# Kernel tuning notes

Hardware: AMD Instinct MI355X
Metric: run time of the kernel (lower is better)

The kernel has to match this reference:

```python
import jax, jax.numpy as jnp
import numpy as np
from jax import lax

R = 3                      # blob_r
S = 2 * R + 1              # 7: maxpool / neighborhood kernel size
THRESH = 0.997
PS_XY = 0.1                # vs_xy
PS_Z = 0.02                # vs_z
ZMIN = -2.0                # zrange[0]
K_PEAKS = 131072           # static upper bound replacing torch.nonzero

_offs = np.arange(S)
_gz, _gy, _gx = np.meshgrid(_offs, _offs, _offs, indexing='ij')  # patch axis order [z,y,x]
GZ = jnp.asarray(_gz.ravel(), dtype=jnp.int32)
GY = jnp.asarray(_gy.ravel(), dtype=jnp.int32)
GX = jnp.asarray(_gx.ravel(), dtype=jnp.int32)
# centroid filters: offsets -r..r along the matching patch axis (matches torch meshgrid layout)
FZ = jnp.asarray((_gz.ravel() - R).astype(np.float32))
FY = jnp.asarray((_gy.ravel() - R).astype(np.float32))
FX = jnp.asarray((_gx.ravel() - R).astype(np.float32))


def setup_inputs() -> dict:
    key = jax.random.key(0)
    pred_vol = jax.random.uniform(key, (1, 1, 128, 512, 512), dtype=jnp.float32)
    return {"pred_vol": pred_vol, "max_peaks": K_PEAKS}


def _forward(pred_vol, max_peaks):
    vol = pred_vol[0, 0]                               # [D,H,W]
    D, H, W = vol.shape
    thr = jnp.where(vol > THRESH, vol, 0.0)
    # MaxPool3d(kernel=2r+1, stride=1, padding=r) == SAME max window (pad with -inf)
    mp = lax.reduce_window(thr, -jnp.inf, lax.max, (S, S, S), (1, 1, 1), [(R, R)] * 3)
    conf = jnp.where((mp > 0.0) & (mp == thr), mp, 0.0)  # local maxima above threshold
    # fixed-size peak extraction (replaces torch.nonzero); zero-valued entries are padding
    vals, idx = lax.top_k(conf.reshape(-1), max_peaks)   # [K], [K]
    z = idx // (H * W)
    y = (idx % (H * W)) // W
    x = idx % W
    padv = jnp.pad(vol, R)                               # ConstantPad3d(r, 0)
    # gather (2r+1)^3 neighborhoods around each peak: [K, S^3]
    patches = padv[z[:, None] + GZ[None, :], y[:, None] + GY[None, :], x[:, None] + GX[None, :]]
    s0 = patches.sum(axis=1)                             # conv3d with ones filter == conf_rec sum
    xloc = jnp.einsum('kp,p->k', patches, FX) / s0
    yloc = jnp.einsum('kp,p->k', patches, FY) / s0
    zloc = jnp.einsum('kp,p->k', patches, FZ) / s0
    xf = x.astype(jnp.float32)
    yf = y.astype(jnp.float32)
    zf = z.astype(jnp.float32)
    xrec = (xf + xloc - (W - 1) / 2.0) * PS_XY
    yrec = (yf + yloc - (H - 1) / 2.0) * PS_XY
    zrec = (zf + zloc + 0.5) * PS_Z + ZMIN
    valid = vals > 0.0
    xyz = jnp.where(valid[:, None], jnp.stack((xrec, yrec, zrec), axis=1), 0.0)  # [K,3]
    out = jnp.concatenate([xyz, vals[:, None]], axis=1)  # [K,4] = (x,y,z,conf), padded rows are 0
    return out, valid


def reference(pred_vol, max_peaks):
    return _forward(pred_vol, max_peaks)
```

## Files before the change

kernel.cpp:

```cpp
#include <hip/hip_runtime.h>

#define DD 128
#define HH 512
#define WW 512
#define NVOX (DD*HH*WW)
#define THRESHV 0.997f
#define KPEAKS 131072
#define PEAK_CAP (1u<<18)
#define NBINS 65536


__global__ void k_init(unsigned* counters, unsigned* hist) {
    unsigned t = blockIdx.x * 1024u + threadIdx.x;
    if (t < 64) counters[t] = 0u;
    if (t < NBINS) hist[t] = 0u;
}

__global__ __launch_bounds__(512, 8)
void k_find(const float4* __restrict__ vol4, const float* __restrict__ vol,
            unsigned* counters, unsigned* hist,
            unsigned long long* keys, float4* psums) {
    __shared__ unsigned lcnt, pcnt, lbase;
    __shared__ unsigned cidx[384];
    __shared__ unsigned long long lbuf[192];
    __shared__ float4 sbuf[192];
    if (threadIdx.x == 0) { lcnt = 0; pcnt = 0; }
    __syncthreads();

    unsigned t = threadIdx.x;
    unsigned lane = t & 63u;
    unsigned w = t >> 6;
    unsigned blockBase4 = blockIdx.x * 2048u;

    unsigned b4 = blockBase4 + t;
    float4 a0 = vol4[b4];
    float4 a1 = vol4[b4 + 512u];
    float4 a2 = vol4[b4 + 1024u];
    float4 a3 = vol4[b4 + 1536u];
    __builtin_amdgcn_sched_barrier(0);
    unsigned m = 0u;
    m |= (a0.x > THRESHV ? 1u : 0u);
    m |= (a0.y > THRESHV ? 2u : 0u);
    m |= (a0.z > THRESHV ? 4u : 0u);
    m |= (a0.w > THRESHV ? 8u : 0u);
    m |= (a1.x > THRESHV ? 16u : 0u);
    m |= (a1.y > THRESHV ? 32u : 0u);
    m |= (a1.z > THRESHV ? 64u : 0u);
    m |= (a1.w > THRESHV ? 128u : 0u);
    m |= (a2.x > THRESHV ? 256u : 0u);
    m |= (a2.y > THRESHV ? 512u : 0u);
    m |= (a2.z > THRESHV ? 1024u : 0u);
    m |= (a2.w > THRESHV ? 2048u : 0u);
    m |= (a3.x > THRESHV ? 4096u : 0u);
    m |= (a3.y > THRESHV ? 8192u : 0u);
    m |= (a3.z > THRESHV ? 16384u : 0u);
    m |= (a3.w > THRESHV ? 32768u : 0u);
    while (m) {
        int b = __ffs(m) - 1;
        m &= m - 1u;
        unsigned f4 = blockBase4 + (unsigned)(b >> 2) * 512u + t;
        cidx[atomicAdd(&lcnt, 1u) & 383u] = f4 * 4u + (unsigned)(b & 3);
    }
    __syncthreads();

    unsigned n = lcnt > 384u ? 384u : lcnt;
    int dz = (int)lane / 7, dy = (int)lane - dz * 7;
    for (unsigned base = w * 2u; base < n; base += 16u) {
        bool has2 = (base + 1u < n);
        unsigned idxA = cidx[base];
        unsigned idxB = has2 ? cidx[base + 1u] : idxA;
        int zA = idxA >> 18, yA = (idxA >> 9) & 511, xA = idxA & 511;
        int zB = idxB >> 18, yB = (idxB >> 9) & 511, xB = idxB & 511;
        int nzA = zA + dz - 3, nyA = yA + dy - 3;
        int nzB = zB + dz - 3, nyB = yB + dy - 3;
        bool rowokA = (lane < 49) && ((unsigned)nzA < DD) && ((unsigned)nyA < HH);
        bool rowokB = (lane < 49) && ((unsigned)nzB < DD) && ((unsigned)nyB < HH);
        size_t rbA = rowokA ? (((size_t)(unsigned)nzA << 18) | ((size_t)(unsigned)nyA << 9))
                            : (((size_t)zA << 18) | ((size_t)yA << 9));
        size_t rbB = rowokB ? (((size_t)(unsigned)nzB << 18) | ((size_t)(unsigned)nyB << 9))
                            : (((size_t)zB << 18) | ((size_t)yB << 9));
        float rvA[7], rvB[7];
        bool intAB = (xA >= 3) && (xA <= WW - 4) && (xB >= 3) && (xB <= WW - 4);
        if (intAB) {
            float4 fA0 = *(const float4*)(vol + rbA + (unsigned)(xA - 3));
            float4 fA1 = *(const float4*)(vol + rbA + (unsigned)(xA + 1));
            float4 fB0 = *(const float4*)(vol + rbB + (unsigned)(xB - 3));
            float4 fB1 = *(const float4*)(vol + rbB + (unsigned)(xB + 1));
            rvA[0] = fA0.x; rvA[1] = fA0.y; rvA[2] = fA0.z; rvA[3] = fA0.w;
            rvA[4] = fA1.x; rvA[5] = fA1.y; rvA[6] = fA1.z;
            rvB[0] = fB0.x; rvB[1] = fB0.y; rvB[2] = fB0.z; rvB[3] = fB0.w;
            rvB[4] = fB1.x; rvB[5] = fB1.y; rvB[6] = fB1.z;
        } else {
#pragma unroll
            for (int d = 0; d < 7; d++) {
                int nxA = xA + d - 3;
                bool okA = (unsigned)nxA < WW;
                float va = vol[rbA + (unsigned)(okA ? nxA : xA)];
                rvA[d] = okA ? va : 0.f;
                int nxB = xB + d - 3;
                bool okB = (unsigned)nxB < WW;
                float vb = vol[rbB + (unsigned)(okB ? nxB : xB)];
                rvB[d] = okB ? vb : 0.f;
            }
        }
        if (!rowokA) {
#pragma unroll
            for (int d = 0; d < 7; d++) rvA[d] = 0.f;
        }
        if (!rowokB) {
#pragma unroll
            for (int d = 0; d < 7; d++) rvB[d] = 0.f;
        }
        float centerA = __shfl(rvA[3], 24);
        float centerB = __shfl(rvB[3], 24);

        {
            bool kill = false;
            float s0r = 0.f, sxr = 0.f;
#pragma unroll
            for (int d = 0; d < 7; d++) {
                kill |= rvA[d] > centerA;
                s0r += rvA[d];
                sxr += rvA[d] * (float)(d - 3);
            }
            if (!__any(kill)) {
                float s0 = s0r, sx = sxr;
                float sy = s0r * (float)(dy - 3);
                float sz = s0r * (float)(dz - 3);
                for (int off = 32; off; off >>= 1) {
                    s0 += __shfl_down(s0, off);
                    sx += __shfl_down(sx, off);
                    sy += __shfl_down(sy, off);
                    sz += __shfl_down(sz, off);
                }
                if (lane == 0) {
                    unsigned bits = __float_as_uint(centerA);
                    atomicAdd(&hist[(~bits) & 0xFFFFu], 1u);
                    unsigned li = atomicAdd(&pcnt, 1u);
                    if (li < 192u) {
                        lbuf[li] = ((unsigned long long)bits << 32) | idxA;
                        sbuf[li] = make_float4(s0, sx, sy, sz);
                    }
                }
            }
        }
        if (has2) {
            bool kill = false;
            float s0r = 0.f, sxr = 0.f;
#pragma unroll
            for (int d = 0; d < 7; d++) {
                kill |= rvB[d] > centerB;
                s0r += rvB[d];
                sxr += rvB[d] * (float)(d - 3);
            }
            if (!__any(kill)) {
                float s0 = s0r, sx = sxr;
                float sy = s0r * (float)(dy - 3);
                float sz = s0r * (float)(dz - 3);
                for (int off = 32; off; off >>= 1) {
                    s0 += __shfl_down(s0, off);
                    sx += __shfl_down(sx, off);
                    sy += __shfl_down(sy, off);
                    sz += __shfl_down(sz, off);
                }
                if (lane == 0) {
                    unsigned bits = __float_as_uint(centerB);
                    atomicAdd(&hist[(~bits) & 0xFFFFu], 1u);
                    unsigned li = atomicAdd(&pcnt, 1u);
                    if (li < 192u) {
                        lbuf[li] = ((unsigned long long)bits << 32) | idxB;
                        sbuf[li] = make_float4(s0, sx, sy, sz);
                    }
                }
            }
        }
    }
    __syncthreads();
    if (threadIdx.x == 0) lbase = atomicAdd(&counters[1], pcnt);
    __syncthreads();
    unsigned np = pcnt > 192u ? 192u : pcnt;
    for (unsigned i = threadIdx.x; i < np; i += 512u) {
        unsigned p = lbase + i;
        if (p < PEAK_CAP) { keys[p] = lbuf[i]; psums[p] = sbuf[i]; }
    }
}

__global__ void k_scan_a(const unsigned* __restrict__ hist,
                         unsigned* __restrict__ cursor,
                         unsigned* __restrict__ blocksum) {
    __shared__ unsigned sc[256];
    unsigned t = threadIdx.x, b = blockIdx.x;
    unsigned h = hist[b * 256u + t];
    sc[t] = h;
    __syncthreads();
    for (unsigned off = 1u; off < 256u; off <<= 1) {
        unsigned v = (t >= off) ? sc[t - off] : 0u;
        __syncthreads();
        sc[t] += v;
        __syncthreads();
    }
    cursor[b * 256u + t] = sc[t] - h;
    if (t == 255u) blocksum[b] = sc[255];
}

__global__ void k_scatter(const unsigned* __restrict__ counters,
                          const unsigned long long* __restrict__ keys,
                          const unsigned* __restrict__ blocksum,
                          unsigned* cursor, unsigned long long* sorted,
                          unsigned* sslot,
                          float4* __restrict__ out, float* __restrict__ valid) {
    __shared__ unsigned bs[256];
    unsigned t = threadIdx.x;
    if (t < 256u) bs[t] = blocksum[t];
    __syncthreads();
    for (unsigned off = 1u; off < 256u; off <<= 1) {
        unsigned v = (t < 256u && t >= off) ? bs[t - off] : 0u;
        __syncthreads();
        if (t < 256u) bs[t] += v;
        __syncthreads();
    }
    unsigned np = counters[1]; if (np > PEAK_CAP) np = PEAK_CAP;
    unsigned g = blockIdx.x * 1024u + t;
    if (g < np) {
        unsigned long long key = keys[g];
        unsigned bits = (unsigned)(key >> 32);
        unsigned bin = (~bits) & 0xFFFFu;
        unsigned c = bin >> 8;
        unsigned base_c = (c > 0u) ? bs[c - 1u] : 0u;
        unsigned pos = base_c + atomicAdd(&cursor[bin], 1u);
        if (pos < PEAK_CAP) { sorted[pos] = key; sslot[pos] = g; }
    } else if (g < KPEAKS) {
        out[g] = make_float4(0.f, 0.f, 0.f, 0.f);
        valid[g] = 0.f;
    }
}

__global__ void k_finish(const unsigned* __restrict__ counters,
                         const unsigned long long* __restrict__ sorted,
                         const unsigned* __restrict__ sslot,
                         const float4* __restrict__ psums,
                         float4* __restrict__ out, float* __restrict__ valid) {
    unsigned np = counters[1]; if (np > PEAK_CAP) np = PEAK_CAP;
    unsigned t = blockIdx.x * 1024u + threadIdx.x;
    if (t >= np) return;
    unsigned long long key = sorted[t];
    unsigned bits = (unsigned)(key >> 32);
    unsigned s = t;
    while (s > 0 && (unsigned)(sorted[s - 1] >> 32) == bits) s--;
    unsigned myidx = (unsigned)key;
    unsigned rank = 0, e = s;
    while (e < np) {
        unsigned long long k2 = sorted[e];
        if ((unsigned)(k2 >> 32) != bits) break;
        if ((unsigned)k2 < myidx) rank++;
        e++;
    }
    unsigned row = s + rank;
    if (row >= KPEAKS) return;
    unsigned idx = myidx;
    int z = idx >> 18, y = (idx >> 9) & 511, x = idx & 511;
    float4 ps = psums[sslot[t]];
    float val = __uint_as_float(bits);
    float xloc = ps.y / ps.x, yloc = ps.z / ps.x, zloc = ps.w / ps.x;
    float xr = ((float)x + xloc - (float)(WW - 1) * 0.5f) * 0.1f;
    float yr = ((float)y + yloc - (float)(HH - 1) * 0.5f) * 0.1f;
    float zr = ((float)z + zloc + 0.5f) * 0.02f - 2.0f;
    out[row] = make_float4(xr, yr, zr, val);
    valid[row] = 1.f;
}

extern "C" void kernel_launch(void* const* d_in, const int* in_sizes, int n_in,
                              void* d_out, int out_size, void* d_ws, size_t ws_size,
                              hipStream_t stream) {
    const float* vol = (const float*)d_in[0];

    char* w = (char*)d_ws;
    unsigned* counters = (unsigned*)w;
    unsigned* hist     = (unsigned*)(w + 1024);
    unsigned* cursor   = (unsigned*)(w + 1024 + NBINS * 4);
    char* w2 = w + 1024 + 2 * NBINS * 4;
    unsigned long long* keys   = (unsigned long long*)w2;
    unsigned long long* sorted = keys + PEAK_CAP;
    unsigned* sslot = (unsigned*)(sorted + PEAK_CAP);
    float4*   psums = (float4*)(sslot + PEAK_CAP);
    unsigned* blocksum = (unsigned*)(psums + PEAK_CAP);

    float* out_rows = (float*)d_out;
    float* valid = out_rows + (size_t)KPEAKS * 4;

    k_init<<<NBINS / 1024, 1024, 0, stream>>>(counters, hist);
    k_find<<<NVOX / 8192, 512, 0, stream>>>((const float4*)vol, vol, counters, hist, keys, psums);
    k_scan_a<<<256, 256, 0, stream>>>(hist, cursor, blocksum);
    k_scatter<<<PEAK_CAP / 1024, 1024, 0, stream>>>(counters, keys, blocksum, cursor,
                                                    sorted, sslot,
                                                    (float4*)out_rows, valid);
    k_finish<<<PEAK_CAP / 1024, 1024, 0, stream>>>(counters, sorted, sslot, psums,
                                                   (float4*)out_rows, valid);
}
```

Before: 241.9 us.

## Process candidates per wavefront via ballot, dropping shared-memory staging and block barriers

Each wavefront now handles its own 1024 voxels. Candidates are found with a ballot loop and each one is checked right away, with no shared-memory candidate list, __syncthreads barriers or block-level staging of peaks. Surviving peaks go straight to global memory through a per-peak atomic on the global counter instead of one atomic per block. Blocks shrink to 256 threads and there are twice as many. This removes block-wide stalls so waves with few candidates can retire early. In exchange it adds many more global atomics, and candidates are no longer processed two at a time, which gives up some memory-level parallelism.

```diff
diff --git a/kernel.cpp b/kernel.cpp
--- a/kernel.cpp
+++ b/kernel.cpp
@@ -16,27 +16,20 @@
     if (t < NBINS) hist[t] = 0u;
 }
 
-__global__ __launch_bounds__(512, 8)
+__global__ __launch_bounds__(256, 8)
 void k_find(const float4* __restrict__ vol4, const float* __restrict__ vol,
             unsigned* counters, unsigned* hist,
             unsigned long long* keys, float4* psums) {
-    __shared__ unsigned lcnt, pcnt, lbase;
-    __shared__ unsigned cidx[384];
-    __shared__ unsigned long long lbuf[192];
-    __shared__ float4 sbuf[192];
-    if (threadIdx.x == 0) { lcnt = 0; pcnt = 0; }
-    __syncthreads();
-
     unsigned t = threadIdx.x;
     unsigned lane = t & 63u;
     unsigned w = t >> 6;
-    unsigned blockBase4 = blockIdx.x * 2048u;
-
-    unsigned b4 = blockBase4 + t;
-    float4 a0 = vol4[b4];
-    float4 a1 = vol4[b4 + 512u];
-    float4 a2 = vol4[b4 + 1024u];
-    float4 a3 = vol4[b4 + 1536u];
+    unsigned wb4 = blockIdx.x * 1024u + w * 256u;
+    int dz = (int)lane / 7, dy = (int)lane - dz * 7;
+
+    float4 a0 = vol4[wb4 + lane];
+    float4 a1 = vol4[wb4 + 64u + lane];
+    float4 a2 = vol4[wb4 + 128u + lane];
+    float4 a3 = vol4[wb4 + 192u + lane];
     __builtin_amdgcn_sched_barrier(0);
     unsigned m = 0u;
     m |= (a0.x > THRESHV ? 1u : 0u);
@@ -55,133 +48,72 @@
     m |= (a3.y > THRESHV ? 8192u : 0u);
     m |= (a3.z > THRESHV ? 16384u : 0u);
     m |= (a3.w > THRESHV ? 32768u : 0u);
-    while (m) {
-        int b = __ffs(m) - 1;
-        m &= m - 1u;
-        unsigned f4 = blockBase4 + (unsigned)(b >> 2) * 512u + t;
-        cidx[atomicAdd(&lcnt, 1u) & 383u] = f4 * 4u + (unsigned)(b & 3);
-    }
-    __syncthreads();
-
-    unsigned n = lcnt > 384u ? 384u : lcnt;
-    int dz = (int)lane / 7, dy = (int)lane - dz * 7;
-    for (unsigned base = w * 2u; base < n; base += 16u) {
-        bool has2 = (base + 1u < n);
-        unsigned idxA = cidx[base];
-        unsigned idxB = has2 ? cidx[base + 1u] : idxA;
-        int zA = idxA >> 18, yA = (idxA >> 9) & 511, xA = idxA & 511;
-        int zB = idxB >> 18, yB = (idxB >> 9) & 511, xB = idxB & 511;
-        int nzA = zA + dz - 3, nyA = yA + dy - 3;
-        int nzB = zB + dz - 3, nyB = yB + dy - 3;
-        bool rowokA = (lane < 49) && ((unsigned)nzA < DD) && ((unsigned)nyA < HH);
-        bool rowokB = (lane < 49) && ((unsigned)nzB < DD) && ((unsigned)nyB < HH);
-        size_t rbA = rowokA ? (((size_t)(unsigned)nzA << 18) | ((size_t)(unsigned)nyA << 9))
-                            : (((size_t)zA << 18) | ((size_t)yA << 9));
-        size_t rbB = rowokB ? (((size_t)(unsigned)nzB << 18) | ((size_t)(unsigned)nyB << 9))
-                            : (((size_t)zB << 18) | ((size_t)yB << 9));
-        float rvA[7], rvB[7];
-        bool intAB = (xA >= 3) && (xA <= WW - 4) && (xB >= 3) && (xB <= WW - 4);
-        if (intAB) {
-            float4 fA0 = *(const float4*)(vol + rbA + (unsigned)(xA - 3));
-            float4 fA1 = *(const float4*)(vol + rbA + (unsigned)(xA + 1));
-            float4 fB0 = *(const float4*)(vol + rbB + (unsigned)(xB - 3));
-            float4 fB1 = *(const float4*)(vol + rbB + (unsigned)(xB + 1));
-            rvA[0] = fA0.x; rvA[1] = fA0.y; rvA[2] = fA0.z; rvA[3] = fA0.w;
-            rvA[4] = fA1.x; rvA[5] = fA1.y; rvA[6] = fA1.z;
-            rvB[0] = fB0.x; rvB[1] = fB0.y; rvB[2] = fB0.z; rvB[3] = fB0.w;
-            rvB[4] = fB1.x; rvB[5] = fB1.y; rvB[6] = fB1.z;
+
+    unsigned long long act = __ballot(m != 0u);
+    while (act) {
+        unsigned src = (unsigned)(__ffsll((unsigned long long)act) - 1);
+        unsigned msrc = __shfl(m, (int)src);
+        unsigned b = (unsigned)(__ffs(msrc) - 1);
+        if (lane == src) m &= (m - 1u);
+        unsigned f4 = wb4 + (b >> 2) * 64u + src;
+        unsigned idx = f4 * 4u + (b & 3u);
+
+        int z = (int)(idx >> 18), y = (int)((idx >> 9) & 511), x = (int)(idx & 511);
+        int nz = z + dz - 3, ny = y + dy - 3;
+        bool rowok = (lane < 49) && ((unsigned)nz < DD) && ((unsigned)ny < HH);
+        size_t rb = rowok ? (((size_t)(unsigned)nz << 18) | ((size_t)(unsigned)ny << 9))
+                          : (((size_t)z << 18) | ((size_t)y << 9));
+        float rv[7];
+        bool interior = (x >= 3) && (x <= WW - 4);
+        if (interior) {
+            float4 f0 = *(const float4*)(vol + rb + (unsigned)(x - 3));
+            float4 f1 = *(const float4*)(vol + rb + (unsigned)(x + 1));
+            rv[0] = f0.x; rv[1] = f0.y; rv[2] = f0.z; rv[3] = f0.w;
+            rv[4] = f1.x; rv[5] = f1.y; rv[6] = f1.z;
         } else {
 #pragma unroll
             for (int d = 0; d < 7; d++) {
-                int nxA = xA + d - 3;
-                bool okA = (unsigned)nxA < WW;
-                float va = vol[rbA + (unsigned)(okA ? nxA : xA)];
-                rvA[d] = okA ? va : 0.f;
-                int nxB = xB + d - 3;
-                bool okB = (unsigned)nxB < WW;
-                float vb = vol[rbB + (unsigned)(okB ? nxB : xB)];
-                rvB[d] = okB ? vb : 0.f;
+                int nx = x + d - 3;
+                bool ok = (unsigned)nx < WW;
+                float v = vol[rb + (unsigned)(ok ? nx : x)];
+                rv[d] = ok ? v : 0.f;
             }
         }
-        if (!rowokA) {
+        if (!rowok) {
 #pragma unroll
-            for (int d = 0; d < 7; d++) rvA[d] = 0.f;
-        }
-        if (!rowokB) {
+            for (int d = 0; d < 7; d++) rv[d] = 0.f;
+        }
+        float center = __shfl(rv[3], 24);
+
+        bool kill = false;
+        float s0r = 0.f, sxr = 0.f;
 #pragma unroll
-            for (int d = 0; d < 7; d++) rvB[d] = 0.f;
-        }
-        float centerA = __shfl(rvA[3], 24);
-        float centerB = __shfl(rvB[3], 24);
-
-        {
-            bool kill = false;
-            float s0r = 0.f, sxr = 0.f;
-#pragma unroll
-            for (int d = 0; d < 7; d++) {
-                kill |= rvA[d] > centerA;
-                s0r += rvA[d];
-                sxr += rvA[d] * (float)(d - 3);
+        for (int d = 0; d < 7; d++) {
+            kill |= rv[d] > center;
+            s0r += rv[d];
+            sxr += rv[d] * (float)(d - 3);
+        }
+        if (!__any(kill)) {
+            float s0 = s0r, sx = sxr;
+            float sy = s0r * (float)(dy - 3);
+            float sz = s0r * (float)(dz - 3);
+            for (int off = 32; off; off >>= 1) {
+                s0 += __shfl_down(s0, off);
+                sx += __shfl_down(sx, off);
+                sy += __shfl_down(sy, off);
+                sz += __shfl_down(sz, off);
             }
-            if (!__any(kill)) {
-                float s0 = s0r, sx = sxr;
-                float sy = s0r * (float)(dy - 3);
-                float sz = s0r * (float)(dz - 3);
-                for (int off = 32; off; off >>= 1) {
-                    s0 += __shfl_down(s0, off);
-                    sx += __shfl_down(sx, off);
-                    sy += __shfl_down(sy, off);
-                    sz += __shfl_down(sz, off);
-                }
-                if (lane == 0) {
-                    unsigned bits = __float_as_uint(centerA);
-                    atomicAdd(&hist[(~bits) & 0xFFFFu], 1u);
-                    unsigned li = atomicAdd(&pcnt, 1u);
-                    if (li < 192u) {
-                        lbuf[li] = ((unsigned long long)bits << 32) | idxA;
-                        sbuf[li] = make_float4(s0, sx, sy, sz);
-                    }
+            if (lane == 0) {
+                unsigned bits = __float_as_uint(center);
+                atomicAdd(&hist[(~bits) & 0xFFFFu], 1u);
+                unsigned slot = atomicAdd(&counters[1], 1u);
+                if (slot < PEAK_CAP) {
+                    keys[slot] = ((unsigned long long)bits << 32) | idx;
+                    psums[slot] = make_float4(s0, sx, sy, sz);
                 }
             }
         }
-        if (has2) {
-            bool kill = false;
-            float s0r = 0.f, sxr = 0.f;
-#pragma unroll
-            for (int d = 0; d < 7; d++) {
-                kill |= rvB[d] > centerB;
-                s0r += rvB[d];
-                sxr += rvB[d] * (float)(d - 3);
-            }
-            if (!__any(kill)) {
-                float s0 = s0r, sx = sxr;
-                float sy = s0r * (float)(dy - 3);
-                float sz = s0r * (float)(dz - 3);
-                for (int off = 32; off; off >>= 1) {
-                    s0 += __shfl_down(s0, off);
-                    sx += __shfl_down(sx, off);
-                    sy += __shfl_down(sy, off);
-                    sz += __shfl_down(sz, off);
-                }
-                if (lane == 0) {
-                    unsigned bits = __float_as_uint(centerB);
-                    atomicAdd(&hist[(~bits) & 0xFFFFu], 1u);
-                    unsigned li = atomicAdd(&pcnt, 1u);
-                    if (li < 192u) {
-                        lbuf[li] = ((unsigned long long)bits << 32) | idxB;
-                        sbuf[li] = make_float4(s0, sx, sy, sz);
-                    }
-                }
-            }
-        }
-    }
-    __syncthreads();
-    if (threadIdx.x == 0) lbase = atomicAdd(&counters[1], pcnt);
-    __syncthreads();
-    unsigned np = pcnt > 192u ? 192u : pcnt;
-    for (unsigned i = threadIdx.x; i < np; i += 512u) {
-        unsigned p = lbase + i;
-        if (p < PEAK_CAP) { keys[p] = lbuf[i]; psums[p] = sbuf[i]; }
+        act = __ballot(m != 0u);
     }
 }
 
@@ -289,7 +221,7 @@
     float* valid = out_rows + (size_t)KPEAKS * 4;
 
     k_init<<<NBINS / 1024, 1024, 0, stream>>>(counters, hist);
-    k_find<<<NVOX / 8192, 512, 0, stream>>>((const float4*)vol, vol, counters, hist, keys, psums);
+    k_find<<<NVOX / 4096, 256, 0, stream>>>((const float4*)vol, vol, counters, hist, keys, psums);
     k_scan_a<<<256, 256, 0, stream>>>(hist, cursor, blocksum);
     k_scatter<<<PEAK_CAP / 1024, 1024, 0, stream>>>(counters, keys, blocksum, cursor,
                                                     sorted, sslot,
```

Result: slower. 899.8 us (+272.0%).
